# Performance work log

Measured on AMD Instinct MI355X. Metric: run time of the kernel, lower is better.

The kernel has to match this reference:

```python
import jax, jax.numpy as jnp
import numpy as np

U = 128          # uniform segment extent (operand_extent)
NSEG = 32        # segments per operand (in0, in1, out)
NPATH = 512      # number of paths
BATCH = 2048


def setup_inputs() -> dict:
    key = jax.random.key(0)
    k0, k1, kc, kp0, kp1, kpo = jax.random.split(key, 6)
    x0 = jax.random.normal(k0, (BATCH, NSEG * U), dtype=jnp.float32)
    x1 = jax.random.normal(k1, (BATCH, NSEG * U), dtype=jnp.float32)
    coeffs = jax.random.normal(kc, (NPATH,), dtype=jnp.float32)
    p0 = jax.random.randint(kp0, (NPATH,), 0, NSEG, dtype=jnp.int32)
    p1 = jax.random.randint(kp1, (NPATH,), 0, NSEG, dtype=jnp.int32)
    pout = jax.random.randint(kpo, (NPATH,), 0, NSEG, dtype=jnp.int32)
    return {"x0": x0, "x1": x1, "coeffs": coeffs, "p0": p0, "p1": p1, "pout": pout}


def reference(x0, x1, coeffs, p0, p1, pout):
    # Segmented uniform tensor product, subscripts 'u,u,u':
    # out[b, pout[k], :] += coeffs[k] * x0[b, p0[k], :] * x1[b, p1[k], :]
    B = x0.shape[0]
    x0s = x0.reshape(B, NSEG, U)
    x1s = x1.reshape(B, NSEG, U)
    # gather per-path segments: [B, P, U]
    contrib = x0s[:, p0, :] * x1s[:, p1, :] * coeffs[None, :, None]
    out = jnp.zeros((B, NSEG, U), dtype=x0.dtype).at[:, pout, :].add(contrib)
    return out.reshape(B, NSEG * U)
```

## Files before the change

kernel.cpp:

```cpp
#include <hip/hip_runtime.h>
#include <hip/hip_fp16.h>

#define U 128
#define NSEG 32
#define NPATH 512
#define ROW (NSEG * U)
#define NW 8

struct Meta { unsigned pp; unsigned c2; };
struct WS {
    Meta meta[NPATH];
    int  segstart[NSEG + 1];
    int  wsplit[NW + 1];
};

template <typename T, typename F> __device__ inline T bcast(F v) {
    union { F f; T t; } u; u.f = v; return u.t;
}

__global__ __launch_bounds__(512) void build_csr(const float* __restrict__ coeffs,
                                                 const int* __restrict__ p0,
                                                 const int* __restrict__ p1,
                                                 const int* __restrict__ pout,
                                                 WS* __restrict__ ws) {
    __shared__ int wcnt[NPATH / 64][NSEG];
    __shared__ int wpre[NPATH / 64][NSEG];
    __shared__ int sseg[NSEG + 1];
    __shared__ int stot[NSEG];

    const int k    = threadIdx.x;
    const int lane = k & 63;
    const int wave = k >> 6;

    const int   po = pout[k];
    const int   a0 = p0[k];
    const int   a1 = p1[k];
    const float c  = coeffs[k];

    const unsigned long long lt = (1ull << lane) - 1ull;
    int rank = 0;
    #pragma unroll
    for (int s = 0; s < NSEG; ++s) {
        unsigned long long m = __ballot(po == s);
        if (po == s)  rank = (int)__popcll(m & lt);
        if (lane == s) wcnt[wave][s] = (int)__popcll(m);
    }
    __syncthreads();

    if (k < NSEG) {
        int tot = 0;
        #pragma unroll
        for (int w = 0; w < NPATH / 64; ++w) { wpre[w][k] = tot; tot += wcnt[w][k]; }
        stot[k] = tot;
    }
    __syncthreads();

    if (k < 64) {
        int v = (k < NSEG) ? stot[k] : 0;
        int inc = v;
        #pragma unroll
        for (int d = 1; d < 64; d <<= 1) {
            int t = __shfl_up(inc, d, 64);
            if (k >= d) inc += t;
        }
        int excl = inc - v;
        if (k < NSEG) sseg[k] = excl;
        if (k == NSEG - 1) sseg[NSEG] = excl + v;
    }
    __syncthreads();

    {
        const __half   h  = __float2half_rn(c);
        const __half2  h2 = __halves2half2(h, h);
        Meta m;
        m.pp = (unsigned)a0 | ((unsigned)a1 << 16);
        m.c2 = bcast<unsigned>(h2);
        ws->meta[sseg[po] + wpre[wave][po] + rank] = m;
    }
    if (k <= NSEG) ws->segstart[k] = sseg[k];

    if (k < 64) {
        #pragma unroll
        for (int w = 1; w < NW; ++w) {
            const int target = (NPATH * w) / NW;
            int key;
            if (k <= NSEG) {
                int d = sseg[k] - target; if (d < 0) d = -d;
                key = (d << 6) | k;
            } else key = 0x7fffffff;
            #pragma unroll
            for (int m = 32; m >= 1; m >>= 1) {
                int o = __shfl_xor(key, m, 64);
                key = (o < key) ? o : key;
            }
            if (k == 0) ws->wsplit[w] = key & 63;
        }
        if (k == 0) { ws->wsplit[0] = 0; ws->wsplit[NW] = NSEG; }
    }
}

__global__ __launch_bounds__(512) void tp_kernel(const float* __restrict__ x0,
                                                 const float* __restrict__ x1,
                                                 const WS* __restrict__ ws,
                                                 float* __restrict__ out) {
    __shared__ __align__(16) __half xh[2 * ROW];
    __shared__ Meta smeta[NPATH];
    __shared__ int  sseg[NSEG + 1];
    __shared__ int  ssplit[NW + 1];

    const int b   = blockIdx.x;
    const int tid = threadIdx.x;

    {
        const float4* g0 = reinterpret_cast<const float4*>(x0 + (size_t)b * ROW);
        const float4* g1 = reinterpret_cast<const float4*>(x1 + (size_t)b * ROW);
        #pragma unroll
        for (int j = 0; j < (ROW / 4) / 512; ++j) {
            const int e = tid + j * 512;
            const float4 v0 = g0[e];
            const float4 v1 = g1[e];
            uint2 h0, h1;
            h0.x = bcast<unsigned>(__float22half2_rn(make_float2(v0.x, v0.y)));
            h0.y = bcast<unsigned>(__float22half2_rn(make_float2(v0.z, v0.w)));
            h1.x = bcast<unsigned>(__float22half2_rn(make_float2(v1.x, v1.y)));
            h1.y = bcast<unsigned>(__float22half2_rn(make_float2(v1.z, v1.w)));
            *reinterpret_cast<uint2*>(&xh[e * 4])       = h0;
            *reinterpret_cast<uint2*>(&xh[ROW + e * 4]) = h1;
        }
    }
    if (tid < NPATH / 2)
        reinterpret_cast<float4*>(smeta)[tid] =
            reinterpret_cast<const float4*>(ws->meta)[tid];
    if (tid < NSEG + 1) sseg[tid] = ws->segstart[tid];
    if (tid < NW + 1)   ssplit[tid] = ws->wsplit[tid];
    __syncthreads();

    const int wave = tid >> 6;
    const int lane = tid & 63;
    const int half = lane >> 5;
    const int sub  = lane & 31;

    const int sBeg = __builtin_amdgcn_readfirstlane(ssplit[wave]);
    const int sEnd = __builtin_amdgcn_readfirstlane(ssplit[wave + 1]);

    float* outrow = out + (size_t)b * ROW;
    const __half2 zero2 = __halves2half2(__float2half_rn(0.f), __float2half_rn(0.f));

    for (int s = sBeg; s < sEnd; ++s) {
        const int jb = __builtin_amdgcn_readfirstlane(sseg[s]);
        const int je = __builtin_amdgcn_readfirstlane(sseg[s + 1]);
        __half2 aA0 = zero2, aA1 = zero2;
        __half2 aB0 = zero2, aB1 = zero2;
        int j = jb;
        for (; j + 3 < je; j += 4) {
            const Meta mA = smeta[j + half];
            const Meta mB = smeta[j + 2 + half];
            const int oA0 = (int)(mA.pp & 0xffffu) << 7;
            const int oA1 = (int)(mA.pp >> 16)     << 7;
            const int oB0 = (int)(mB.pp & 0xffffu) << 7;
            const int oB1 = (int)(mB.pp >> 16)     << 7;
            const uint2 uA = *reinterpret_cast<const uint2*>(&xh[oA0 + sub * 4]);
            const uint2 wA = *reinterpret_cast<const uint2*>(&xh[ROW + oA1 + sub * 4]);
            const uint2 uB = *reinterpret_cast<const uint2*>(&xh[oB0 + sub * 4]);
            const uint2 wB = *reinterpret_cast<const uint2*>(&xh[ROW + oB1 + sub * 4]);
            const __half2 cA = bcast<__half2>(mA.c2);
            const __half2 cB = bcast<__half2>(mB.c2);
            aA0 = __hfma2(__hmul2(bcast<__half2>(uA.x), bcast<__half2>(wA.x)), cA, aA0);
            aA1 = __hfma2(__hmul2(bcast<__half2>(uA.y), bcast<__half2>(wA.y)), cA, aA1);
            aB0 = __hfma2(__hmul2(bcast<__half2>(uB.x), bcast<__half2>(wB.x)), cB, aB0);
            aB1 = __hfma2(__hmul2(bcast<__half2>(uB.y), bcast<__half2>(wB.y)), cB, aB1);
        }
        for (; j + 1 < je; j += 2) {
            const Meta m = smeta[j + half];
            const int o0 = (int)(m.pp & 0xffffu) << 7;
            const int o1 = (int)(m.pp >> 16)     << 7;
            const uint2 u = *reinterpret_cast<const uint2*>(&xh[o0 + sub * 4]);
            const uint2 w = *reinterpret_cast<const uint2*>(&xh[ROW + o1 + sub * 4]);
            const __half2 c = bcast<__half2>(m.c2);
            aA0 = __hfma2(__hmul2(bcast<__half2>(u.x), bcast<__half2>(w.x)), c, aA0);
            aA1 = __hfma2(__hmul2(bcast<__half2>(u.y), bcast<__half2>(w.y)), c, aA1);
        }
        if (j < je) {
            const Meta m = smeta[j];
            const int o0 = (int)(m.pp & 0xffffu) << 7;
            const int o1 = (int)(m.pp >> 16)     << 7;
            const uint2 u = *reinterpret_cast<const uint2*>(&xh[o0 + sub * 4]);
            const uint2 w = *reinterpret_cast<const uint2*>(&xh[ROW + o1 + sub * 4]);
            const __half2 c = (half == 0) ? bcast<__half2>(m.c2) : zero2;
            aA0 = __hfma2(__hmul2(bcast<__half2>(u.x), bcast<__half2>(w.x)), c, aA0);
            aA1 = __hfma2(__hmul2(bcast<__half2>(u.y), bcast<__half2>(w.y)), c, aA1);
        }
        const float2 f0a = __half22float2(aA0), f0b = __half22float2(aB0);
        const float2 f1a = __half22float2(aA1), f1b = __half22float2(aB1);
        float4 a;
        a.x = f0a.x + f0b.x;
        a.y = f0a.y + f0b.y;
        a.z = f1a.x + f1b.x;
        a.w = f1a.y + f1b.y;
        a.x += __shfl_xor(a.x, 32, 64);
        a.y += __shfl_xor(a.y, 32, 64);
        a.z += __shfl_xor(a.z, 32, 64);
        a.w += __shfl_xor(a.w, 32, 64);
        if (half == 0)
            reinterpret_cast<float4*>(outrow + s * U)[sub] = a;
    }
}

extern "C" void kernel_launch(void* const* d_in, const int* in_sizes, int n_in,
                              void* d_out, int out_size, void* d_ws, size_t ws_size,
                              hipStream_t stream) {
    const float* x0     = (const float*)d_in[0];
    const float* x1     = (const float*)d_in[1];
    const float* coeffs = (const float*)d_in[2];
    const int*   p0     = (const int*)d_in[3];
    const int*   p1     = (const int*)d_in[4];
    const int*   pout   = (const int*)d_in[5];
    float* out = (float*)d_out;
    WS* ws = (WS*)d_ws;

    build_csr<<<1, 512, 0, stream>>>(coeffs, p0, p1, pout, ws);
    tp_kernel<<<2048, 512, 0, stream>>>(x0, x1, ws, out);
}
```

Baseline: 34.74 us.

## Process two rows per block with prefetch, padded LDS layout, 16-byte gathers

Each block now handles two batch rows. The second row's global loads are issued up front and written to a second LDS buffer after the first row is computed, so load latency overlaps compute. Segments are padded to 272 bytes to reduce bank conflicts. Lanes are split into four groups of 16 that gather 16-byte uint4 chunks, and per-segment path counts are padded to multiples of 4 with zero-coefficient metadata to remove tail handling. This costs more registers for the prefetched data and a larger LDS footprint, which may reduce occupancy.

After: 43.75 us. 1.26x slower.

```diff
diff --git a/kernel.cpp b/kernel.cpp
--- a/kernel.cpp
+++ b/kernel.cpp
@@ -6,10 +6,16 @@
 #define NPATH 512
 #define ROW (NSEG * U)
 #define NW 8
+#define NMETA 640
+#define SEGB 272
+#define XH1 (NSEG * SEGB)
+#define ROWBUF (2 * NSEG * SEGB)
+#define ROWS_PER_BLOCK 2
+#define NBLK 1024
 
 struct Meta { unsigned pp; unsigned c2; };
 struct WS {
-    Meta meta[NPATH];
+    Meta meta[NMETA];
     int  segstart[NSEG + 1];
     int  wsplit[NW + 1];
 };
@@ -37,6 +43,8 @@
     const int   a1 = p1[k];
     const float c  = coeffs[k];
 
+    for (int i = k; i < NMETA; i += 512) { Meta z; z.pp = 0u; z.c2 = 0u; ws->meta[i] = z; }
+
     const unsigned long long lt = (1ull << lane) - 1ull;
     int rank = 0;
     #pragma unroll
@@ -56,7 +64,7 @@
     __syncthreads();
 
     if (k < 64) {
-        int v = (k < NSEG) ? stot[k] : 0;
+        int v = (k < NSEG) ? ((stot[k] + 3) & ~3) : 0;
         int inc = v;
         #pragma unroll
         for (int d = 1; d < 64; d <<= 1) {
@@ -80,9 +88,10 @@
     if (k <= NSEG) ws->segstart[k] = sseg[k];
 
     if (k < 64) {
+        const int tot = sseg[NSEG];
         #pragma unroll
         for (int w = 1; w < NW; ++w) {
-            const int target = (NPATH * w) / NW;
+            const int target = (tot * w) / NW;
             int key;
             if (k <= NSEG) {
                 int d = sseg[k] - target; if (d < 0) d = -d;
@@ -99,36 +108,43 @@
     }
 }
 
+__device__ inline uint2 cvt4(float4 v) {
+    uint2 r;
+    r.x = bcast<unsigned>(__float22half2_rn(make_float2(v.x, v.y)));
+    r.y = bcast<unsigned>(__float22half2_rn(make_float2(v.z, v.w)));
+    return r;
+}
+
 __global__ __launch_bounds__(512) void tp_kernel(const float* __restrict__ x0,
                                                  const float* __restrict__ x1,
                                                  const WS* __restrict__ ws,
                                                  float* __restrict__ out) {
-    __shared__ __align__(16) __half xh[2 * ROW];
-    __shared__ Meta smeta[NPATH];
+    __shared__ __align__(16) char xbuf[2][ROWBUF];
+    __shared__ Meta smeta[NMETA];
     __shared__ int  sseg[NSEG + 1];
     __shared__ int  ssplit[NW + 1];
 
-    const int b   = blockIdx.x;
     const int tid = threadIdx.x;
-
-    {
-        const float4* g0 = reinterpret_cast<const float4*>(x0 + (size_t)b * ROW);
-        const float4* g1 = reinterpret_cast<const float4*>(x1 + (size_t)b * ROW);
-        #pragma unroll
-        for (int j = 0; j < (ROW / 4) / 512; ++j) {
-            const int e = tid + j * 512;
-            const float4 v0 = g0[e];
-            const float4 v1 = g1[e];
-            uint2 h0, h1;
-            h0.x = bcast<unsigned>(__float22half2_rn(make_float2(v0.x, v0.y)));
-            h0.y = bcast<unsigned>(__float22half2_rn(make_float2(v0.z, v0.w)));
-            h1.x = bcast<unsigned>(__float22half2_rn(make_float2(v1.x, v1.y)));
-            h1.y = bcast<unsigned>(__float22half2_rn(make_float2(v1.z, v1.w)));
-            *reinterpret_cast<uint2*>(&xh[e * 4])       = h0;
-            *reinterpret_cast<uint2*>(&xh[ROW + e * 4]) = h1;
-        }
-    }
-    if (tid < NPATH / 2)
+    const int b0  = blockIdx.x * ROWS_PER_BLOCK;
+
+    const float4* g00 = reinterpret_cast<const float4*>(x0 + (size_t)b0 * ROW);
+    const float4* g01 = reinterpret_cast<const float4*>(x1 + (size_t)b0 * ROW);
+    const float4* g10 = reinterpret_cast<const float4*>(x0 + (size_t)(b0 + 1) * ROW);
+    const float4* g11 = reinterpret_cast<const float4*>(x1 + (size_t)(b0 + 1) * ROW);
+    const float4 A0 = g00[tid], A1 = g00[tid + 512];
+    const float4 A2 = g01[tid], A3 = g01[tid + 512];
+    const float4 B0 = g10[tid], B1 = g10[tid + 512];
+    const float4 B2 = g11[tid], B3 = g11[tid + 512];
+
+    auto wr = [&](int buf, int e, const float4& vx0, const float4& vx1) {
+        const int off = (e >> 5) * SEGB + (e & 31) * 8;
+        *reinterpret_cast<uint2*>(&xbuf[buf][off])       = cvt4(vx0);
+        *reinterpret_cast<uint2*>(&xbuf[buf][XH1 + off]) = cvt4(vx1);
+    };
+    wr(0, tid, A0, A2);
+    wr(0, tid + 512, A1, A3);
+
+    if (tid < NMETA / 2)
         reinterpret_cast<float4*>(smeta)[tid] =
             reinterpret_cast<const float4*>(ws->meta)[tid];
     if (tid < NSEG + 1) sseg[tid] = ws->segstart[tid];
@@ -137,72 +153,82 @@
 
     const int wave = tid >> 6;
     const int lane = tid & 63;
-    const int half = lane >> 5;
-    const int sub  = lane & 31;
+    const int g    = lane >> 4;
+    const int t    = lane & 15;
 
     const int sBeg = __builtin_amdgcn_readfirstlane(ssplit[wave]);
     const int sEnd = __builtin_amdgcn_readfirstlane(ssplit[wave + 1]);
-
-    float* outrow = out + (size_t)b * ROW;
-    const __half2 zero2 = __halves2half2(__float2half_rn(0.f), __float2half_rn(0.f));
-
-    for (int s = sBeg; s < sEnd; ++s) {
-        const int jb = __builtin_amdgcn_readfirstlane(sseg[s]);
-        const int je = __builtin_amdgcn_readfirstlane(sseg[s + 1]);
-        __half2 aA0 = zero2, aA1 = zero2;
-        __half2 aB0 = zero2, aB1 = zero2;
-        int j = jb;
-        for (; j + 3 < je; j += 4) {
-            const Meta mA = smeta[j + half];
-            const Meta mB = smeta[j + 2 + half];
-            const int oA0 = (int)(mA.pp & 0xffffu) << 7;
-            const int oA1 = (int)(mA.pp >> 16)     << 7;
-            const int oB0 = (int)(mB.pp & 0xffffu) << 7;
-            const int oB1 = (int)(mB.pp >> 16)     << 7;
-            const uint2 uA = *reinterpret_cast<const uint2*>(&xh[oA0 + sub * 4]);
-            const uint2 wA = *reinterpret_cast<const uint2*>(&xh[ROW + oA1 + sub * 4]);
-            const uint2 uB = *reinterpret_cast<const uint2*>(&xh[oB0 + sub * 4]);
-            const uint2 wB = *reinterpret_cast<const uint2*>(&xh[ROW + oB1 + sub * 4]);
-            const __half2 cA = bcast<__half2>(mA.c2);
-            const __half2 cB = bcast<__half2>(mB.c2);
-            aA0 = __hfma2(__hmul2(bcast<__half2>(uA.x), bcast<__half2>(wA.x)), cA, aA0);
-            aA1 = __hfma2(__hmul2(bcast<__half2>(uA.y), bcast<__half2>(wA.y)), cA, aA1);
-            aB0 = __hfma2(__hmul2(bcast<__half2>(uB.x), bcast<__half2>(wB.x)), cB, aB0);
-            aB1 = __hfma2(__hmul2(bcast<__half2>(uB.y), bcast<__half2>(wB.y)), cB, aB1);
-        }
-        for (; j + 1 < je; j += 2) {
-            const Meta m = smeta[j + half];
-            const int o0 = (int)(m.pp & 0xffffu) << 7;
-            const int o1 = (int)(m.pp >> 16)     << 7;
-            const uint2 u = *reinterpret_cast<const uint2*>(&xh[o0 + sub * 4]);
-            const uint2 w = *reinterpret_cast<const uint2*>(&xh[ROW + o1 + sub * 4]);
-            const __half2 c = bcast<__half2>(m.c2);
-            aA0 = __hfma2(__hmul2(bcast<__half2>(u.x), bcast<__half2>(w.x)), c, aA0);
-            aA1 = __hfma2(__hmul2(bcast<__half2>(u.y), bcast<__half2>(w.y)), c, aA1);
-        }
-        if (j < je) {
-            const Meta m = smeta[j];
-            const int o0 = (int)(m.pp & 0xffffu) << 7;
-            const int o1 = (int)(m.pp >> 16)     << 7;
-            const uint2 u = *reinterpret_cast<const uint2*>(&xh[o0 + sub * 4]);
-            const uint2 w = *reinterpret_cast<const uint2*>(&xh[ROW + o1 + sub * 4]);
-            const __half2 c = (half == 0) ? bcast<__half2>(m.c2) : zero2;
-            aA0 = __hfma2(__hmul2(bcast<__half2>(u.x), bcast<__half2>(w.x)), c, aA0);
-            aA1 = __hfma2(__hmul2(bcast<__half2>(u.y), bcast<__half2>(w.y)), c, aA1);
-        }
-        const float2 f0a = __half22float2(aA0), f0b = __half22float2(aB0);
-        const float2 f1a = __half22float2(aA1), f1b = __half22float2(aB1);
-        float4 a;
-        a.x = f0a.x + f0b.x;
-        a.y = f0a.y + f0b.y;
-        a.z = f1a.x + f1b.x;
-        a.w = f1a.y + f1b.y;
-        a.x += __shfl_xor(a.x, 32, 64);
-        a.y += __shfl_xor(a.y, 32, 64);
-        a.z += __shfl_xor(a.z, 32, 64);
-        a.w += __shfl_xor(a.w, 32, 64);
-        if (half == 0)
-            reinterpret_cast<float4*>(outrow + s * U)[sub] = a;
+    const int tOff = t << 4;
+
+    #pragma unroll
+    for (int r = 0; r < ROWS_PER_BLOCK; ++r) {
+        const char* xb = xbuf[r];
+        float* outrow = out + (size_t)(b0 + r) * ROW;
+
+        for (int s = sBeg; s < sEnd; ++s) {
+            const int jb = __builtin_amdgcn_readfirstlane(sseg[s]);
+            const int je = __builtin_amdgcn_readfirstlane(sseg[s + 1]);
+            __half2 aA0, aA1, aA2, aA3, aB0, aB1, aB2, aB3;
+            aA0 = aA1 = aA2 = aA3 = aB0 = aB1 = aB2 = aB3 =
+                bcast<__half2>(0u);
+            int j = jb;
+            for (; j + 7 < je; j += 8) {
+                const Meta mA = smeta[j + g];
+                const Meta mB = smeta[j + 4 + g];
+                const uint4 uA = *reinterpret_cast<const uint4*>(
+                    &xb[(int)(mA.pp & 0xffffu) * SEGB + tOff]);
+                const uint4 wA = *reinterpret_cast<const uint4*>(
+                    &xb[XH1 + (int)(mA.pp >> 16) * SEGB + tOff]);
+                const uint4 uB = *reinterpret_cast<const uint4*>(
+                    &xb[(int)(mB.pp & 0xffffu) * SEGB + tOff]);
+                const uint4 wB = *reinterpret_cast<const uint4*>(
+                    &xb[XH1 + (int)(mB.pp >> 16) * SEGB + tOff]);
+                const __half2 cA = bcast<__half2>(mA.c2);
+                const __half2 cB = bcast<__half2>(mB.c2);
+                aA0 = __hfma2(__hmul2(bcast<__half2>(uA.x), bcast<__half2>(wA.x)), cA, aA0);
+                aA1 = __hfma2(__hmul2(bcast<__half2>(uA.y), bcast<__half2>(wA.y)), cA, aA1);
+                aA2 = __hfma2(__hmul2(bcast<__half2>(uA.z), bcast<__half2>(wA.z)), cA, aA2);
+                aA3 = __hfma2(__hmul2(bcast<__half2>(uA.w), bcast<__half2>(wA.w)), cA, aA3);
+                aB0 = __hfma2(__hmul2(bcast<__half2>(uB.x), bcast<__half2>(wB.x)), cB, aB0);
+                aB1 = __hfma2(__hmul2(bcast<__half2>(uB.y), bcast<__half2>(wB.y)), cB, aB1);
+                aB2 = __hfma2(__hmul2(bcast<__half2>(uB.z), bcast<__half2>(wB.z)), cB, aB2);
+                aB3 = __hfma2(__hmul2(bcast<__half2>(uB.w), bcast<__half2>(wB.w)), cB, aB3);
+            }
+            if (j < je) {
+                const Meta m = smeta[j + g];
+                const uint4 u = *reinterpret_cast<const uint4*>(
+                    &xb[(int)(m.pp & 0xffffu) * SEGB + tOff]);
+                const uint4 w = *reinterpret_cast<const uint4*>(
+                    &xb[XH1 + (int)(m.pp >> 16) * SEGB + tOff]);
+                const __half2 c = bcast<__half2>(m.c2);
+                aA0 = __hfma2(__hmul2(bcast<__half2>(u.x), bcast<__half2>(w.x)), c, aA0);
+                aA1 = __hfma2(__hmul2(bcast<__half2>(u.y), bcast<__half2>(w.y)), c, aA1);
+                aA2 = __hfma2(__hmul2(bcast<__half2>(u.z), bcast<__half2>(w.z)), c, aA2);
+                aA3 = __hfma2(__hmul2(bcast<__half2>(u.w), bcast<__half2>(w.w)), c, aA3);
+            }
+            const float2 r0 = __half22float2(__hadd2(aA0, aB0));
+            const float2 r1 = __half22float2(__hadd2(aA1, aB1));
+            const float2 r2 = __half22float2(__hadd2(aA2, aB2));
+            const float2 r3 = __half22float2(__hadd2(aA3, aB3));
+            float v[8] = { r0.x, r0.y, r1.x, r1.y, r2.x, r2.y, r3.x, r3.y };
+            #pragma unroll
+            for (int i = 0; i < 8; ++i) {
+                v[i] += __shfl_xor(v[i], 16, 64);
+                v[i] += __shfl_xor(v[i], 32, 64);
+            }
+            if (g < 2) {
+                float4 o;
+                o.x = v[g * 4 + 0]; o.y = v[g * 4 + 1];
+                o.z = v[g * 4 + 2]; o.w = v[g * 4 + 3];
+                reinterpret_cast<float4*>(outrow + s * U)[t * 2 + g] = o;
+            }
+        }
+
+        if (r == 0) {
+            wr(1, tid, B0, B2);
+            wr(1, tid + 512, B1, B3);
+            __syncthreads();
+        }
     }
 }
 
@@ -219,5 +245,5 @@
     WS* ws = (WS*)d_ws;
 
     build_csr<<<1, 512, 0, stream>>>(coeffs, p0, p1, pout, ws);
-    tp_kernel<<<2048, 512, 0, stream>>>(x0, x1, ws, out);
-}
+    tp_kernel<<<NBLK, 512, 0, stream>>>(x0, x1, ws, out);
+}
```
